# Performance work log

Measured on AMD Instinct MI355X. Metric: run time of the kernel, lower is better.

Reference implementation:

```python
import jax, jax.numpy as jnp
import numpy as np

B, N, D = 8, 1024, 256
H, U = 8, 64  # num_heads, units per head


def setup_inputs() -> dict:
    key = jax.random.key(0)
    ks = jax.random.split(key, 8)
    X = jax.random.normal(ks[0], (B, N, D), dtype=jnp.float32)
    A = (jax.random.uniform(ks[1], (B, N, N)) < 0.1).astype(jnp.float32)
    A = jnp.maximum(A, jnp.eye(N, dtype=jnp.float32)[None])
    s = 1.0 / np.sqrt(D)
    kernel = jax.random.normal(ks[2], (D, H * U), dtype=jnp.float32) * s
    kernel_residual = jax.random.normal(ks[3], (D, H * U), dtype=jnp.float32) * s
    su = 1.0 / np.sqrt(U)
    attn_kernel_self = jax.random.normal(ks[4], (H, U, 1), dtype=jnp.float32) * su
    attn_kernel_neighs = jax.random.normal(ks[5], (H, U, 1), dtype=jnp.float32) * su
    bias = jnp.zeros((H * U,), dtype=jnp.float32)
    return {
        "X": X, "A": A,
        "kernel": kernel, "kernel_residual": kernel_residual,
        "attn_kernel_self": attn_kernel_self,
        "attn_kernel_neighs": attn_kernel_neighs,
        "bias": bias,
    }


def reference(X, A, kernel, kernel_residual, attn_kernel_self, attn_kernel_neighs, bias):
    # feature projections: [B,N,H*U]
    features = X @ kernel
    features_residual = X @ kernel_residual
    f = features.reshape(B, N, H, U)  # bnhu
    # additive attention logits per head
    attn_self = jnp.einsum('bnhu,hu->bnh', f, attn_kernel_self[..., 0])
    attn_neigh = jnp.einsum('bnhu,hu->bnh', f, attn_kernel_neighs[..., 0])
    dense = attn_self[:, :, None, :] + attn_neigh[:, None, :, :]  # b n k h
    dense = jax.nn.leaky_relu(dense, negative_slope=0.2)
    # mask non-edges, softmax over neighbor axis k
    dense = dense + (-1e10) * (1.0 - A)[..., None]
    attn_coef = jax.nn.softmax(dense, axis=2)
    # (dropout is identity in inference mode)
    node_features = jnp.einsum('bnkh,bkhu->bnhu', attn_coef, f)
    node_features = node_features.reshape(B, N, H * U) + features_residual + bias
    # head_reduction == 'concat' -> keep [B,N,H*U]
    return jax.nn.relu(node_features)
```

## Files before the change

### kernel.cpp

```cpp
#include <hip/hip_runtime.h>
#include <stdint.h>


typedef __attribute__((ext_vector_type(8))) short short8;
typedef __attribute__((ext_vector_type(4))) float f32x4;

__device__ __forceinline__ unsigned short f32_to_bf16(float f) {
    unsigned int u = __float_as_uint(f);
    u = (u + 0x7fffu + ((u >> 16) & 1u)) >> 16;
    return (unsigned short)u;
}
__device__ __forceinline__ float bf16_to_f32(unsigned short s) {
    return __uint_as_float(((unsigned int)s) << 16);
}
__device__ __forceinline__ void load_lds16(const unsigned short* g, unsigned short* l) {
    __builtin_amdgcn_global_load_lds(
        (const __attribute__((address_space(1))) unsigned int*)g,
        (__attribute__((address_space(3))) unsigned int*)l, 16, 0, 0);
}

__global__ __launch_bounds__(256) void pack_a(const float* __restrict__ X,
                                              unsigned short* __restrict__ Abig) {
    const int idx = blockIdx.x * 256 + threadIdx.x;
    const int m  = idx >> 6;
    const int kg = (idx & 63) << 2;
    float4 x = *(const float4*)&X[m * 256 + kg];
    const float xs[4] = {x.x, x.y, x.z, x.w};
    union { unsigned short u[4]; uint64_t q; } hq, lq;
    #pragma unroll
    for (int i = 0; i < 4; i++) {
        unsigned short h = f32_to_bf16(xs[i]);
        hq.u[i] = h;
        lq.u[i] = f32_to_bf16(xs[i] - bf16_to_f32(h));
    }
    unsigned short* r = Abig + (size_t)m * 768;
    *(uint64_t*)(r + kg)       = hq.q;
    *(uint64_t*)(r + 256 + kg) = hq.q;
    *(uint64_t*)(r + 512 + kg) = lq.q;
}

__global__ __launch_bounds__(256) void pack_b(const float* __restrict__ Wk,
                                              const float* __restrict__ Wr,
                                              unsigned short* __restrict__ Bpack) {
    const int idx = blockIdx.x * 256 + threadIdx.x;
    const int n = idx / 768;
    const int k = idx - n * 768;
    const float* __restrict__ W = (n < 512) ? Wk : Wr;
    const int nc = n & 511;
    const float w = W[(k & 255) * 512 + nc];
    unsigned short h = f32_to_bf16(w);
    unsigned short o = (k >= 256 && k < 512) ? f32_to_bf16(w - bf16_to_f32(h)) : h;
    Bpack[idx] = o;
}

__global__ __launch_bounds__(512) void attn_ck(const float* __restrict__ kernel,
                                               const float* __restrict__ aks,
                                               const float* __restrict__ akn,
                                               float* __restrict__ ck) {
    const int d = blockIdx.x, j = threadIdx.x;
    const float kv = kernel[d * 512 + j];
    float a = kv * aks[j];
    float b = kv * akn[j];
    #pragma unroll
    for (int m = 32; m; m >>= 1) { a += __shfl_xor(a, m, 64); b += __shfl_xor(b, m, 64); }
    const int lane = j & 63, h = j >> 6;
    if (lane == 0) { ck[d * 16 + h] = a; ck[d * 16 + 8 + h] = b; }
}

__global__ __launch_bounds__(256) void attn_sa(const float* __restrict__ X,
                                               const float* __restrict__ ck,
                                               float* __restrict__ saan) {
    __shared__ __align__(16) float Xs[16][260];
    __shared__ __align__(16) float ckL[4096];
    const int t = threadIdx.x, row0 = blockIdx.x * 16;
    #pragma unroll
    for (int i = 0; i < 4; i++) {
        const int q = t + i * 256;
        const int r = q >> 6, c4 = (q & 63) * 4;
        *(float4*)&Xs[r][c4] = *(const float4*)&X[(size_t)(row0 + r) * 256 + c4];
        *(float4*)&ckL[q * 4] = *(const float4*)&ck[q * 4];
    }
    __syncthreads();
    const int r = t >> 4, o = t & 15;
    float acc = 0.f;
    #pragma unroll 4
    for (int d = 0; d < 256; d++) acc = fmaf(Xs[r][d], ckL[d * 16 + o], acc);
    saan[(size_t)(row0 + r) * 16 + o] = acc;
}

#define GK 768
__global__ __launch_bounds__(256) void gemm_bf16(const unsigned short* __restrict__ Ab,
                                                 const unsigned short* __restrict__ Bp,
                                                 unsigned short* __restrict__ featT,
                                                 float* __restrict__ outr) {
    __shared__ __align__(16) unsigned short As[128 * 32];
    __shared__ __align__(16) unsigned short Bs[128 * 32];
    const int tid = threadIdx.x;
    const int lane = tid & 63, wave = tid >> 6;
    const int wr = wave >> 1, wc = wave & 1;
    const int m0 = blockIdx.x * 128, n0 = blockIdx.y * 128;
    const int l15 = lane & 15, lhi = lane >> 4;

    f32x4 acc[4][4] = {};

    for (int k0 = 0; k0 < GK; k0 += 32) {
        #pragma unroll
        for (int i = 0; i < 2; i++) {
            const int s = tid + i * 256;
            const int row = s >> 2, kc = (s & 3) * 8;
            load_lds16(Ab + (size_t)(m0 + row) * GK + k0 + kc, &As[s * 8]);
            load_lds16(Bp + (size_t)(n0 + row) * GK + k0 + kc, &Bs[s * 8]);
        }
        asm volatile("s_waitcnt vmcnt(0)" ::: "memory");
        __syncthreads();
        short8 a[4], b[4];
        #pragma unroll
        for (int mi = 0; mi < 4; mi++)
            a[mi] = *(const short8*)&As[(wr * 64 + mi * 16 + l15) * 32 + lhi * 8];
        #pragma unroll
        for (int ni = 0; ni < 4; ni++)
            b[ni] = *(const short8*)&Bs[(wc * 64 + ni * 16 + l15) * 32 + lhi * 8];
        #pragma unroll
        for (int mi = 0; mi < 4; mi++)
            #pragma unroll
            for (int ni = 0; ni < 4; ni++)
                acc[mi][ni] = __builtin_amdgcn_mfma_f32_16x16x32_bf16(a[mi], b[ni], acc[mi][ni], 0, 0, 0);
        __syncthreads();
    }

    if (n0 < 512) {
        #pragma unroll
        for (int mi = 0; mi < 4; mi++)
            #pragma unroll
            for (int ni = 0; ni < 4; ni++) {
                const int col = n0 + wc * 64 + ni * 16 + l15;
                const int rbase = m0 + wr * 64 + mi * 16 + lhi * 4;
                const int bb = rbase >> 10, nl = rbase & 1023;
                union { unsigned short u[4]; uint64_t q; } pk;
                #pragma unroll
                for (int r = 0; r < 4; r++) pk.u[r] = f32_to_bf16(acc[mi][ni][r]);
                *(uint64_t*)&featT[(size_t)bb * 524288 + (size_t)col * 1024 + nl] = pk.q;
            }
    } else {
        #pragma unroll
        for (int mi = 0; mi < 4; mi++)
            #pragma unroll
            for (int ni = 0; ni < 4; ni++) {
                const int col = (n0 - 512) + wc * 64 + ni * 16 + l15;
                const int rbase = m0 + wr * 64 + mi * 16 + lhi * 4;
                #pragma unroll
                for (int r = 0; r < 4; r++)
                    outr[(size_t)(rbase + r) * 512 + col] = acc[mi][ni][r];
            }
    }
}

__global__ __launch_bounds__(512) void gat_mfma(
    const float* __restrict__ A, const unsigned short* __restrict__ featT,
    const float* __restrict__ saan, const float* __restrict__ bias,
    float* __restrict__ out) {
    __shared__ float an_s[1024][9];

    const int blk = blockIdx.x;
    const int b  = blk & 7;
    const int n0 = (blk >> 3) * 16;
    const int t = threadIdx.x;
    const int w = t >> 6;
    const int lane = t & 63;
    const int l15 = lane & 15, lhi = lane >> 4;

    #pragma unroll
    for (int i = 0; i < 4; i++) {
        const int idx = i * 512 + t;
        const int k = idx >> 1, half = (idx & 1) * 4;
        float4 v = *(const float4*)&saan[(size_t)(b * 1024 + k) * 16 + 8 + half];
        an_s[k][half + 0] = v.x; an_s[k][half + 1] = v.y;
        an_s[k][half + 2] = v.z; an_s[k][half + 3] = v.w;
    }
    const float as_r = saan[(size_t)(b * 1024 + n0 + l15) * 16 + w];

    short8 ones;
    #pragma unroll
    for (int i = 0; i < 8; i++) ones[i] = (short)0x3F80;

    f32x4 acc[4] = {};
    f32x4 accs = {};
    const unsigned short* __restrict__ fT = featT + (size_t)b * 524288;
    const float* __restrict__ Arow = A + (size_t)(b * 1024 + n0 + l15) * 1024;

    __syncthreads();

    for (int k0 = 0; k0 < 1024; k0 += 32) {
        float4 a0 = *(const float4*)&Arow[k0 + lhi * 8];
        float4 a1 = *(const float4*)&Arow[k0 + lhi * 8 + 4];
        const float av[8] = {a0.x, a0.y, a0.z, a0.w, a1.x, a1.y, a1.z, a1.w};

        union { short8 s8; unsigned int u32[4]; } pa;
        #pragma unroll
        for (int q = 0; q < 4; q++) {
            float pv[2];
            #pragma unroll
            for (int d = 0; d < 2; d++) {
                const int j = q * 2 + d;
                float x = as_r + an_s[k0 + lhi * 8 + j][w];
                x = fmaxf(x, 0.2f * x);
                const float e = __expf(x);
                pv[d] = (av[j] > 0.5f) ? e : 0.f;
            }
            unsigned int pk;
            asm("v_cvt_pk_bf16_f32 %0, %1, %2" : "=v"(pk) : "v"(pv[0]), "v"(pv[1]));
            pa.u32[q] = pk;
        }
        short8 bf[4];
        #pragma unroll
        for (int ni = 0; ni < 4; ni++)
            bf[ni] = *(const short8*)&fT[(size_t)(w * 64 + ni * 16 + l15) * 1024 + k0 + lhi * 8];
        #pragma unroll
        for (int ni = 0; ni < 4; ni++)
            acc[ni] = __builtin_amdgcn_mfma_f32_16x16x32_bf16(pa.s8, bf[ni], acc[ni], 0, 0, 0);
        accs = __builtin_amdgcn_mfma_f32_16x16x32_bf16(pa.s8, ones, accs, 0, 0, 0);
    }

    #pragma unroll
    for (int r = 0; r < 4; r++) {
        const int row_l = lhi * 4 + r;
        const float iv = 1.0f / accs[r];
        const size_t rb = (size_t)(b * 1024 + n0 + row_l) * 512 + w * 64;
        #pragma unroll
        for (int ni = 0; ni < 4; ni++) {
            const int col = ni * 16 + l15;
            const float v = fmaf(acc[ni][r], iv, out[rb + col] + bias[w * 64 + col]);
            out[rb + col] = fmaxf(v, 0.f);
        }
    }
}

extern "C" void kernel_launch(void* const* d_in, const int* in_sizes, int n_in,
                              void* d_out, int out_size, void* d_ws, size_t ws_size,
                              hipStream_t stream) {
    const float* X    = (const float*)d_in[0];
    const float* A    = (const float*)d_in[1];
    const float* Wk   = (const float*)d_in[2];
    const float* Wr   = (const float*)d_in[3];
    const float* aks  = (const float*)d_in[4];
    const float* akn  = (const float*)d_in[5];
    const float* bias = (const float*)d_in[6];
    float* out = (float*)d_out;

    unsigned short* featT = (unsigned short*)d_ws;
    float* saan = (float*)(featT + (size_t)8 * 512 * 1024);
    float* ck   = saan + (size_t)8192 * 16;
    unsigned short* Abig  = (unsigned short*)(ck + 4096);
    unsigned short* Bpack = Abig + (size_t)8192 * 768;

    pack_a<<<2048, 256, 0, stream>>>(X, Abig);
    pack_b<<<3072, 256, 0, stream>>>(Wk, Wr, Bpack);
    attn_ck<<<256, 512, 0, stream>>>(Wk, aks, akn, ck);
    attn_sa<<<512, 256, 0, stream>>>(X, ck, saan);
    gemm_bf16<<<dim3(64, 8), 256, 0, stream>>>(Abig, Bpack, featT, out);
    gat_mfma<<<512, 512, 0, stream>>>(A, featT, saan, bias, out);
}
```

Measured before the change: 218.2 us.

## Restructure GAT attention kernel with bitmask adjacency, transposed logits and exp2

The attention kernel now handles 32 rows per block with 1024 threads. Each block first packs its adjacency rows into an LDS bitmask, replacing the per-iteration float loads of A. Neighbor logits are written transposed per head, so they can be read as float4 from LDS. The logits are prescaled by log2(e) so the hardware exp2 replaces expf. Together these cut redundant A traffic and LDS bank conflicts, at the cost of fewer blocks and larger LDS use per block.

```diff
diff --git a/kernel.cpp b/kernel.cpp
--- a/kernel.cpp
+++ b/kernel.cpp
@@ -64,12 +64,16 @@
     #pragma unroll
     for (int m = 32; m; m >>= 1) { a += __shfl_xor(a, m, 64); b += __shfl_xor(b, m, 64); }
     const int lane = j & 63, h = j >> 6;
-    if (lane == 0) { ck[d * 16 + h] = a; ck[d * 16 + 8 + h] = b; }
+    if (lane == 0) {
+        ck[d * 16 + h]     = a * 1.4426950408889634f;
+        ck[d * 16 + 8 + h] = b * 1.4426950408889634f;
+    }
 }
 
 __global__ __launch_bounds__(256) void attn_sa(const float* __restrict__ X,
                                                const float* __restrict__ ck,
-                                               float* __restrict__ saan) {
+                                               float* __restrict__ as_g,
+                                               float* __restrict__ an_Tg) {
     __shared__ __align__(16) float Xs[16][260];
     __shared__ __align__(16) float ckL[4096];
     const int t = threadIdx.x, row0 = blockIdx.x * 16;
@@ -85,7 +89,11 @@
     float acc = 0.f;
     #pragma unroll 4
     for (int d = 0; d < 256; d++) acc = fmaf(Xs[r][d], ckL[d * 16 + o], acc);
-    saan[(size_t)(row0 + r) * 16 + o] = acc;
+    const int grow = row0 + r;
+    if (o < 8)
+        as_g[(size_t)grow * 8 + o] = acc;
+    else
+        an_Tg[((size_t)(grow >> 10) * 8 + (o - 8)) * 1024 + (grow & 1023)] = acc;
 }
 
 #define GK 768
@@ -155,29 +163,43 @@
     }
 }
 
-__global__ __launch_bounds__(512) void gat_mfma(
+__global__ __launch_bounds__(1024) void gat_mfma2(
     const float* __restrict__ A, const unsigned short* __restrict__ featT,
-    const float* __restrict__ saan, const float* __restrict__ bias,
-    float* __restrict__ out) {
-    __shared__ float an_s[1024][9];
+    const float* __restrict__ as_g, const float* __restrict__ an_Tg,
+    const float* __restrict__ bias, float* __restrict__ out) {
+    __shared__ float an_T[8192];
+    __shared__ unsigned int maskA[32][33];
 
     const int blk = blockIdx.x;
     const int b  = blk & 7;
-    const int n0 = (blk >> 3) * 16;
+    const int n0 = (blk >> 3) * 32;
     const int t = threadIdx.x;
-    const int w = t >> 6;
-    const int lane = t & 63;
-    const int l15 = lane & 15, lhi = lane >> 4;
-
-    #pragma unroll
-    for (int i = 0; i < 4; i++) {
-        const int idx = i * 512 + t;
-        const int k = idx >> 1, half = (idx & 1) * 4;
-        float4 v = *(const float4*)&saan[(size_t)(b * 1024 + k) * 16 + 8 + half];
-        an_s[k][half + 0] = v.x; an_s[k][half + 1] = v.y;
-        an_s[k][half + 2] = v.z; an_s[k][half + 3] = v.w;
-    }
-    const float as_r = saan[(size_t)(b * 1024 + n0 + l15) * 16 + w];
+    const int w16 = t >> 6;
+    const int h = w16 & 7, half = w16 >> 3;
+    const int lane = t & 63, l15 = lane & 15, lhi = lane >> 4;
+
+    {
+        const float* __restrict__ src = an_Tg + (size_t)b * 8192;
+        *(float4*)&an_T[t * 8]     = *(const float4*)&src[t * 8];
+        *(float4*)&an_T[t * 8 + 4] = *(const float4*)&src[t * 8 + 4];
+    }
+    {
+        const int row = t >> 5, wd = t & 31;
+        const float* __restrict__ ap = A + ((size_t)(b << 10) + n0 + row) * 1024 + wd * 32;
+        unsigned int m = 0;
+        #pragma unroll
+        for (int i = 0; i < 8; i++) {
+            float4 v = *(const float4*)&ap[i * 4];
+            if (v.x > 0.5f) m |= 1u << (i * 4 + 0);
+            if (v.y > 0.5f) m |= 1u << (i * 4 + 1);
+            if (v.z > 0.5f) m |= 1u << (i * 4 + 2);
+            if (v.w > 0.5f) m |= 1u << (i * 4 + 3);
+        }
+        maskA[row][wd] = m;
+    }
+
+    const int arow = half * 16 + l15;
+    const float as_r = as_g[((size_t)(b << 10) + n0 + arow) * 8 + h];
 
     short8 ones;
     #pragma unroll
@@ -185,15 +207,17 @@
 
     f32x4 acc[4] = {};
     f32x4 accs = {};
-    const unsigned short* __restrict__ fT = featT + (size_t)b * 524288;
-    const float* __restrict__ Arow = A + (size_t)(b * 1024 + n0 + l15) * 1024;
+    const unsigned short* __restrict__ fT =
+        featT + (size_t)b * 524288 + (size_t)(h * 64) * 1024;
 
     __syncthreads();
 
     for (int k0 = 0; k0 < 1024; k0 += 32) {
-        float4 a0 = *(const float4*)&Arow[k0 + lhi * 8];
-        float4 a1 = *(const float4*)&Arow[k0 + lhi * 8 + 4];
-        const float av[8] = {a0.x, a0.y, a0.z, a0.w, a1.x, a1.y, a1.z, a1.w};
+        const unsigned int m = maskA[arow][k0 >> 5];
+        const float* __restrict__ anp = &an_T[h * 1024 + k0 + lhi * 8];
+        float4 an0 = *(const float4*)&anp[0];
+        float4 an1 = *(const float4*)&anp[4];
+        const float av[8] = {an0.x, an0.y, an0.z, an0.w, an1.x, an1.y, an1.z, an1.w};
 
         union { short8 s8; unsigned int u32[4]; } pa;
         #pragma unroll
@@ -202,10 +226,10 @@
             #pragma unroll
             for (int d = 0; d < 2; d++) {
                 const int j = q * 2 + d;
-                float x = as_r + an_s[k0 + lhi * 8 + j][w];
+                float x = as_r + av[j];
                 x = fmaxf(x, 0.2f * x);
-                const float e = __expf(x);
-                pv[d] = (av[j] > 0.5f) ? e : 0.f;
+                const float e = __builtin_amdgcn_exp2f(x);
+                pv[d] = (m & (1u << (lhi * 8 + j))) ? e : 0.f;
             }
             unsigned int pk;
             asm("v_cvt_pk_bf16_f32 %0, %1, %2" : "=v"(pk) : "v"(pv[0]), "v"(pv[1]));
@@ -214,7 +238,7 @@
         short8 bf[4];
         #pragma unroll
         for (int ni = 0; ni < 4; ni++)
-            bf[ni] = *(const short8*)&fT[(size_t)(w * 64 + ni * 16 + l15) * 1024 + k0 + lhi * 8];
+            bf[ni] = *(const short8*)&fT[(size_t)(ni * 16 + l15) * 1024 + k0 + lhi * 8];
         #pragma unroll
         for (int ni = 0; ni < 4; ni++)
             acc[ni] = __builtin_amdgcn_mfma_f32_16x16x32_bf16(pa.s8, bf[ni], acc[ni], 0, 0, 0);
@@ -223,13 +247,13 @@
 
     #pragma unroll
     for (int r = 0; r < 4; r++) {
-        const int row_l = lhi * 4 + r;
+        const int row_l = half * 16 + lhi * 4 + r;
         const float iv = 1.0f / accs[r];
-        const size_t rb = (size_t)(b * 1024 + n0 + row_l) * 512 + w * 64;
+        const size_t rb = ((size_t)(b << 10) + n0 + row_l) * 512 + h * 64;
         #pragma unroll
         for (int ni = 0; ni < 4; ni++) {
             const int col = ni * 16 + l15;
-            const float v = fmaf(acc[ni][r], iv, out[rb + col] + bias[w * 64 + col]);
+            const float v = fmaf(acc[ni][r], iv, out[rb + col] + bias[h * 64 + col]);
             out[rb + col] = fmaxf(v, 0.f);
         }
     }
@@ -248,15 +272,16 @@
     float* out = (float*)d_out;
 
     unsigned short* featT = (unsigned short*)d_ws;
-    float* saan = (float*)(featT + (size_t)8 * 512 * 1024);
-    float* ck   = saan + (size_t)8192 * 16;
+    float* as_g  = (float*)(featT + (size_t)8 * 512 * 1024);
+    float* an_Tg = as_g + 65536;
+    float* ck    = an_Tg + 65536;
     unsigned short* Abig  = (unsigned short*)(ck + 4096);
     unsigned short* Bpack = Abig + (size_t)8192 * 768;
 
     pack_a<<<2048, 256, 0, stream>>>(X, Abig);
     pack_b<<<3072, 256, 0, stream>>>(Wk, Wr, Bpack);
     attn_ck<<<256, 512, 0, stream>>>(Wk, aks, akn, ck);
-    attn_sa<<<512, 256, 0, stream>>>(X, ck, saan);
+    attn_sa<<<512, 256, 0, stream>>>(X, ck, as_g, an_Tg);
     gemm_bf16<<<dim3(64, 8), 256, 0, stream>>>(Abig, Bpack, featT, out);
-    gat_mfma<<<512, 512, 0, stream>>>(A, featT, saan, bias, out);
-}
+    gat_mfma2<<<256, 1024, 0, stream>>>(A, featT, as_g, an_Tg, bias, out);
+}
```

After: 193.8 us. 11.2% less time.
